# Performance work log

Hardware: AMD Instinct MI355X
Metric: run time of the kernel (lower is better)

## Reference

```python
import jax, jax.numpy as jnp
from jax import lax
from jax.experimental.ode import odeint
import numpy as np

INPUT_DIM, HIDDEN_DIM, LATENT_DIM, OUTPUT_DIM = 6, 64, 16, 1
RTOL, ATOL = 1e-3, 1e-4
NOISE_STD = 0.0  # model_noise=0 -> deterministic drift, faithful to relu(W z + b) + 0
B, T = 2048, 512


def _init(key, shape, fan_in):
    bound = 1.0 / np.sqrt(fan_in)
    return jax.random.uniform(key, shape, jnp.float32, -bound, bound)


def setup_inputs() -> dict:
    key = jax.random.key(0)
    ks = jax.random.split(key, 18)
    inp = {
        "x": jax.random.normal(ks[0], (B, T, INPUT_DIM), jnp.float32),
        # encoder GRU (input 6 -> hidden 64), torch layout: W_ih [3H, D], W_hh [3H, H]
        "enc_Wih": _init(ks[1], (3 * HIDDEN_DIM, INPUT_DIM), HIDDEN_DIM),
        "enc_Whh": _init(ks[2], (3 * HIDDEN_DIM, HIDDEN_DIM), HIDDEN_DIM),
        "enc_bih": _init(ks[3], (3 * HIDDEN_DIM,), HIDDEN_DIM),
        "enc_bhh": _init(ks[4], (3 * HIDDEN_DIM,), HIDDEN_DIM),
        "fc_mu_W": _init(ks[5], (LATENT_DIM, HIDDEN_DIM), HIDDEN_DIM),
        "fc_mu_b": _init(ks[6], (LATENT_DIM,), HIDDEN_DIM),
        "fc_lv_W": _init(ks[7], (LATENT_DIM, HIDDEN_DIM), HIDDEN_DIM),
        "fc_lv_b": _init(ks[8], (LATENT_DIM,), HIDDEN_DIM),
        # latent SDE drift linear 16 -> 16
        "ode_W": _init(ks[9], (LATENT_DIM, LATENT_DIM), LATENT_DIM),
        "ode_b": _init(ks[10], (LATENT_DIM,), LATENT_DIM),
        # decoder fc 16 -> 64, then GRU (input 64 -> hidden 1)
        "dec_fc_W": _init(ks[11], (HIDDEN_DIM, LATENT_DIM), LATENT_DIM),
        "dec_fc_b": _init(ks[12], (HIDDEN_DIM,), LATENT_DIM),
        "dec_Wih": _init(ks[13], (3 * OUTPUT_DIM, HIDDEN_DIM), OUTPUT_DIM),
        "dec_Whh": _init(ks[14], (3 * OUTPUT_DIM, OUTPUT_DIM), OUTPUT_DIM),
        "dec_bih": _init(ks[15], (3 * OUTPUT_DIM,), OUTPUT_DIM),
        "dec_bhh": _init(ks[16], (3 * OUTPUT_DIM,), OUTPUT_DIM),
    }
    return inp


def _gru_cell(h, x_gates, Whh, bhh):
    # x_gates: precomputed x @ Wih.T + bih, shape [B, 3H]; h: [B, H]
    h_gates = h @ Whh.T + bhh
    xr, xz, xn = jnp.split(x_gates, 3, axis=-1)
    hr, hz, hn = jnp.split(h_gates, 3, axis=-1)
    r = jax.nn.sigmoid(xr + hr)
    zg = jax.nn.sigmoid(xz + hz)
    n = jnp.tanh(xn + r * hn)
    return (1.0 - zg) * n + zg * h


def _forward(x, enc_Wih, enc_Whh, enc_bih, enc_bhh, fc_mu_W, fc_mu_b,
             fc_lv_W, fc_lv_b, ode_W, ode_b, dec_fc_W, dec_fc_b,
             dec_Wih, dec_Whh, dec_bih, dec_bhh):
    Bsz, Tlen, _ = x.shape
    # ---- encoder GRU, keep only last hidden state ----
    xg = jnp.einsum('btd,gd->btg', x, enc_Wih) + enc_bih  # [B,T,3H]
    h0 = jnp.zeros((Bsz, HIDDEN_DIM), x.dtype)
    def enc_step(h, xt):
        return _gru_cell(h, xt, enc_Whh, enc_bhh), None
    hT, _ = lax.scan(enc_step, h0, jnp.swapaxes(xg, 0, 1))
    mu = hT @ fc_mu_W.T + fc_mu_b          # [B,16]
    log_var = hT @ fc_lv_W.T + fc_lv_b     # [B,16]
    # deterministic reparam exactly as source: z = mu + sqrt(exp(log_var))
    z0 = mu + jnp.exp(0.5 * log_var)
    # ---- dopri5 adaptive integration of dz/dt = relu(W z + b) on t in [0,1] ----
    def drift(z, t):
        return jax.nn.relu(z @ ode_W.T + ode_b)
    ts = jnp.linspace(0.0, 1.0, 10)
    zs = odeint(drift, z0, ts, rtol=RTOL, atol=ATOL)
    z = zs[-1]                              # [B,16]
    # ---- decoder: relu(fc1), repeat over time, GRU(64->1) ----
    zd = jax.nn.relu(z @ dec_fc_W.T + dec_fc_b)            # [B,64]
    xg_dec = zd @ dec_Wih.T + dec_bih                       # same every step, [B,3]
    hd0 = jnp.zeros((Bsz, OUTPUT_DIM), x.dtype)
    def dec_step(h, _):
        h = _gru_cell(h, xg_dec, dec_Whh, dec_bhh)
        return h, h
    _, outs = lax.scan(dec_step, hd0, None, length=Tlen)    # [T,B,1]
    x_recon = jnp.swapaxes(outs, 0, 1)                      # [B,T,1]
    return x_recon, mu, log_var


def reference(x, enc_Wih, enc_Whh, enc_bih, enc_bhh, fc_mu_W, fc_mu_b,
              fc_lv_W, fc_lv_b, ode_W, ode_b, dec_fc_W, dec_fc_b,
              dec_Wih, dec_Whh, dec_bih, dec_bhh):
    return _forward(x, enc_Wih, enc_Whh, enc_bih, enc_bhh, fc_mu_W, fc_mu_b,
                    fc_lv_W, fc_lv_b, ode_W, ode_b, dec_fc_W, dec_fc_b,
                    dec_Wih, dec_Whh, dec_bih, dec_bhh)
```

## Files before the change

### kernel.cpp

```cpp
#include <hip/hip_runtime.h>
#include <math.h>

#define B_TOTAL 2048
#define T_LEN   512
#define IN_D    6
#define HID     64
#define LAT     16
#define ROWS    4
#define THREADS 256
#define ASTRIDE 104

typedef __attribute__((ext_vector_type(8))) short bfrag;
typedef __attribute__((ext_vector_type(4))) float ffrag;

#if __has_builtin(__builtin_amdgcn_exp2f)
#define EXP2F(x) __builtin_amdgcn_exp2f(x)
#else
#define EXP2F(x) exp2f(x)
#endif
#if __has_builtin(__builtin_amdgcn_rcpf)
#define RCPF(x) __builtin_amdgcn_rcpf(x)
#else
#define RCPF(x) (1.0f / (x))
#endif

__device__ __forceinline__ float fast_sigmoid(float x){
    return RCPF(1.0f + EXP2F(-1.44269504088896340736f * x));
}
__device__ __forceinline__ float fast_tanh(float x){
    return 1.0f - 2.0f * RCPF(EXP2F(2.88539008177792681472f * x) + 1.0f);
}
__device__ __forceinline__ unsigned short f2bf_rne(float f){
    unsigned u = __float_as_uint(f);
    return (unsigned short)((u + 0x7fffu + ((u >> 16) & 1u)) >> 16);
}

extern "C" __global__ void
__attribute__((amdgpu_flat_work_group_size(THREADS, THREADS), amdgpu_waves_per_eu(2, 2)))
glsde_kernel(const float* __restrict__ x,
             const float* __restrict__ eWih, const float* __restrict__ eWhh,
             const float* __restrict__ ebih, const float* __restrict__ ebhh,
             const float* __restrict__ muW,  const float* __restrict__ mub,
             const float* __restrict__ lvW,  const float* __restrict__ lvb,
             const float* __restrict__ oW,   const float* __restrict__ ob,
             const float* __restrict__ dfW,  const float* __restrict__ dfb,
             const float* __restrict__ dWih, const float* __restrict__ dWhh,
             const float* __restrict__ dbih, const float* __restrict__ dbhh,
             float* __restrict__ out)
{
    __shared__ __align__(16) unsigned short xstage[T_LEN][ROWS][8];
    __shared__ __align__(16) unsigned short Abuf[2][16][ASTRIDE];
    __shared__ float hfp[ROWS][HID];
    __shared__ float zsh[ROWS][LAT];
    __shared__ float zdsh[ROWS][HID];
    __shared__ float xgdsh[ROWS][3];

    const int tid  = threadIdx.x;
    const int wave = tid >> 6;
    const int lane = tid & 63;
    const int nloc = lane & 15;
    const int quad = lane >> 4;
    const int mA   = lane & 15;
    const int j    = wave * 16 + nloc;
    const int b0   = blockIdx.x * ROWS;

    const float S1 = 1.44269504088896340736f;
    const float S2 = 2.0f * S1;

    bfrag Br[3], Bz[3], Bnh[2], Bnx;
    {
        const float* wr  = eWhh + (size_t)(      j) * HID;
        const float* wz  = eWhh + (size_t)( 64 + j) * HID;
        const float* wn  = eWhh + (size_t)(128 + j) * HID;
        #pragma unroll
        for (int kt = 0; kt < 2; ++kt){
            const int o = kt * 32 + quad * 8;
            #pragma unroll
            for (int e = 0; e < 8; ++e){
                Br[kt][e]  = (short)f2bf_rne(wr[o+e] * S1);
                Bz[kt][e]  = (short)f2bf_rne(wz[o+e] * S1);
                Bnh[kt][e] = (short)f2bf_rne(wn[o+e] * S2);
            }
        }
        const float* ir  = eWih + (size_t)(      j) * IN_D;
        const float* iz  = eWih + (size_t)( 64 + j) * IN_D;
        const float* inn = eWih + (size_t)(128 + j) * IN_D;
        #pragma unroll
        for (int e = 0; e < 8; ++e){
            bool v = (quad == 0 && e < IN_D);
            Br[2][e] = v ? (short)f2bf_rne(ir[e]  * S1) : (short)0;
            Bz[2][e] = v ? (short)f2bf_rne(iz[e]  * S1) : (short)0;
            Bnx[e]   = v ? (short)f2bf_rne(inn[e] * S2) : (short)0;
        }
    }
    const float bias_r = (ebih[j]      + ebhh[j])      * S1;
    const float bias_z = (ebih[64 + j] + ebhh[64 + j]) * S1;
    const float bihn2  = ebih[128 + j] * S2;
    const float bhhn2  = ebhh[128 + j] * S2;

    {
        unsigned* ap = (unsigned*)Abuf;
        for (int i = tid; i < (int)(sizeof(Abuf) / 4); i += THREADS) ap[i] = 0u;
    }

    for (int idx = tid; idx < T_LEN * ROWS; idx += THREADS){
        const int tt = idx & (T_LEN - 1);
        const int bb = idx >> 9;
        const float* xr = x + (size_t)(b0 + bb) * T_LEN * IN_D + (size_t)tt * IN_D;
        const float2* p2 = (const float2*)xr;
        float2 v0 = p2[0], v1 = p2[1], v2 = p2[2];
        bfrag f;
        f[0] = (short)f2bf_rne(v0.x); f[1] = (short)f2bf_rne(v0.y);
        f[2] = (short)f2bf_rne(v1.x); f[3] = (short)f2bf_rne(v1.y);
        f[4] = (short)f2bf_rne(v2.x); f[5] = (short)f2bf_rne(v2.y);
        f[6] = 0; f[7] = 0;
        *(bfrag*)&xstage[tt][bb][0] = f;
    }
    __syncthreads();

    float hreg = 0.f;

    const unsigned short* xsp = &xstage[0][mA >> 2][0];

    bfrag Ax = *(const bfrag*)(xsp);
    const ffrag FZ = {0.f, 0.f, 0.f, 0.f};

#define GRU_STEP(bufR, bufW, T)                                                    \
    do {                                                                           \
        const unsigned short* ah_ = &bufR[mA][0];                                  \
        bfrag Ah0 = *(const bfrag*)(ah_ + 0  + quad * 8);                          \
        bfrag Ah1 = *(const bfrag*)(ah_ + 32 + quad * 8);                          \
        int tn_ = (T) + 1; if (tn_ >= T_LEN) tn_ = T_LEN - 1;                      \
        bfrag AxN = *(const bfrag*)(xsp + (size_t)tn_ * (ROWS * 8));               \
        ffrag aRx = {bias_r, 0.f, 0.f, 0.f};                                       \
        ffrag aZx = {bias_z, 0.f, 0.f, 0.f};                                       \
        ffrag aXx = {bihn2,  0.f, 0.f, 0.f};                                       \
        ffrag aR0 = FZ, aR1 = FZ, aZ0 = FZ, aZ1 = FZ;                              \
        ffrag aH0 = FZ, aH1 = FZ;                                                  \
                       \
        aRx = __builtin_amdgcn_mfma_f32_16x16x32_bf16(Ax,  Br[2],  aRx, 0,0,0);    \
        aZx = __builtin_amdgcn_mfma_f32_16x16x32_bf16(Ax,  Bz[2],  aZx, 0,0,0);    \
        aXx = __builtin_amdgcn_mfma_f32_16x16x32_bf16(Ax,  Bnx,    aXx, 0,0,0);    \
        aR0 = __builtin_amdgcn_mfma_f32_16x16x32_bf16(Ah0, Br[0],  aR0, 0,0,0);    \
        aZ0 = __builtin_amdgcn_mfma_f32_16x16x32_bf16(Ah0, Bz[0],  aZ0, 0,0,0);    \
        aH0 = __builtin_amdgcn_mfma_f32_16x16x32_bf16(Ah0, Bnh[0], aH0, 0,0,0);    \
        aR1 = __builtin_amdgcn_mfma_f32_16x16x32_bf16(Ah1, Br[1],  aR1, 0,0,0);    \
        aZ1 = __builtin_amdgcn_mfma_f32_16x16x32_bf16(Ah1, Bz[1],  aZ1, 0,0,0);    \
        aH1 = __builtin_amdgcn_mfma_f32_16x16x32_bf16(Ah1, Bnh[1], aH1, 0,0,0);    \
        float pr = aRx[0] + (aR0[0] + aR1[0]);                                     \
        float pz = aZx[0] + (aZ0[0] + aZ1[0]);                                     \
        float ph = bhhn2  + (aH0[0] + aH1[0]);                                     \
        float rg = RCPF(1.0f + EXP2F(-pr));                                        \
        float zg = RCPF(1.0f + EXP2F(-pz));                                        \
        float yy = aXx[0] + rg * ph;                                               \
        float ng = 1.0f - 2.0f * RCPF(EXP2F(yy) + 1.0f);                           \
        float hn = (1.0f - zg) * ng + zg * hreg;                                   \
        hreg = hn;                                                                 \
        bufW[quad * 4][j] = f2bf_rne(hn);                                          \
        Ax = AxN;                                                                  \
        __syncthreads();                                                           \
    } while (0)

    for (int t = 0; t < T_LEN; t += 2){
        GRU_STEP(Abuf[0], Abuf[1], t);
        GRU_STEP(Abuf[1], Abuf[0], t + 1);
    }
#undef GRU_STEP

    hfp[quad][j] = hreg;
    __syncthreads();

    const int zrow = tid >> 4, zi = tid & 15;
    float z0v = 0.0f;
    if (tid < ROWS * LAT){
        float am = mub[zi], al = lvb[zi];
        const float4* pm = (const float4*)(muW + (size_t)zi * HID);
        const float4* pq = (const float4*)(lvW + (size_t)zi * HID);
        const float4* ph = (const float4*)(&hfp[zrow][0]);
        #pragma unroll
        for (int q = 0; q < 16; ++q){
            float4 wm = pm[q], wl = pq[q], hv = ph[q];
            am += wm.x*hv.x + wm.y*hv.y + wm.z*hv.z + wm.w*hv.w;
            al += wl.x*hv.x + wl.y*hv.y + wl.z*hv.z + wl.w*hv.w;
        }
        const size_t muBase = (size_t)B_TOTAL * T_LEN;
        out[muBase + (size_t)(b0 + zrow) * LAT + zi] = am;
        out[muBase + (size_t)B_TOTAL * LAT + (size_t)(b0 + zrow) * LAT + zi] = al;
        z0v = am + __expf(0.5f * al);
    }

    if (tid < ROWS * LAT){
        float ows[16];
        {
            const float4* pw = (const float4*)(oW + (size_t)zi * LAT);
            #pragma unroll
            for (int q = 0; q < 4; ++q){
                float4 w = pw[q];
                ows[4*q+0] = w.x; ows[4*q+1] = w.y; ows[4*q+2] = w.z; ows[4*q+3] = w.w;
            }
        }
        const float obv = ob[zi];
        float z = z0v;
        const float hstep = 1.0f / 24.0f;
        for (int s = 0; s < 24; ++s){
            float y, k1, k2, k3, k4;
            y = z;
            { float acc = obv;
              #pragma unroll
              for (int jj = 0; jj < 16; ++jj){ float yj = __shfl(y, jj, 16); acc = fmaf(ows[jj], yj, acc); }
              k1 = fmaxf(acc, 0.0f); }
            y = z + 0.5f * hstep * k1;
            { float acc = obv;
              #pragma unroll
              for (int jj = 0; jj < 16; ++jj){ float yj = __shfl(y, jj, 16); acc = fmaf(ows[jj], yj, acc); }
              k2 = fmaxf(acc, 0.0f); }
            y = z + 0.5f * hstep * k2;
            { float acc = obv;
              #pragma unroll
              for (int jj = 0; jj < 16; ++jj){ float yj = __shfl(y, jj, 16); acc = fmaf(ows[jj], yj, acc); }
              k3 = fmaxf(acc, 0.0f); }
            y = z + hstep * k3;
            { float acc = obv;
              #pragma unroll
              for (int jj = 0; jj < 16; ++jj){ float yj = __shfl(y, jj, 16); acc = fmaf(ows[jj], yj, acc); }
              k4 = fmaxf(acc, 0.0f); }
            z += (hstep / 6.0f) * (k1 + 2.0f*k2 + 2.0f*k3 + k4);
        }
        zsh[zrow][zi] = z;
    }
    __syncthreads();

    for (int idx = tid; idx < ROWS * HID; idx += THREADS){
        const int row = idx >> 6, o = idx & 63;
        float acc = dfb[o];
        const float4* pw = (const float4*)(dfW + (size_t)o * LAT);
        const float4* pz = (const float4*)(&zsh[row][0]);
        #pragma unroll
        for (int q = 0; q < 4; ++q){
            float4 w = pw[q], zv = pz[q];
            acc += w.x*zv.x + w.y*zv.y + w.z*zv.z + w.w*zv.w;
        }
        zdsh[row][o] = fmaxf(acc, 0.0f);
    }
    __syncthreads();

    if (tid < ROWS * 3){
        const int row = tid / 3, gg = tid % 3;
        float acc = dbih[gg];
        const float4* pw = (const float4*)(dWih + (size_t)gg * HID);
        const float4* pz = (const float4*)(&zdsh[row][0]);
        #pragma unroll
        for (int q = 0; q < 16; ++q){
            float4 w = pw[q], zv = pz[q];
            acc += w.x*zv.x + w.y*zv.y + w.z*zv.z + w.w*zv.w;
        }
        xgdsh[row][gg] = acc;
    }
    __syncthreads();

    if (tid < ROWS){
        const int row = tid;
        const float xr = xgdsh[row][0], xz = xgdsh[row][1], xn = xgdsh[row][2];
        const float A0 = dWhh[0], A1 = dWhh[1], A2 = dWhh[2];
        const float c0 = dbhh[0], c1 = dbhh[1], c2 = dbhh[2];
        float* orow = out + (size_t)(b0 + row) * T_LEN;
        float h = 0.0f;
        float ob4[4];
        for (int t = 0; t < T_LEN; ++t){
            float rr = fast_sigmoid(xr + A0 * h + c0);
            float zz = fast_sigmoid(xz + A1 * h + c1);
            float nn = fast_tanh(xn + rr * (A2 * h + c2));
            h = (1.0f - zz) * nn + zz * h;
            ob4[t & 3] = h;
            if ((t & 3) == 3) *(float4*)(orow + (t - 3)) = *(float4*)ob4;
        }
    }
}

extern "C" void kernel_launch(void* const* d_in, const int* in_sizes, int n_in,
                              void* d_out, int out_size, void* d_ws, size_t ws_size,
                              hipStream_t stream){
    glsde_kernel<<<B_TOTAL / ROWS, THREADS, 0, stream>>>(
        (const float*)d_in[0],  (const float*)d_in[1],  (const float*)d_in[2],
        (const float*)d_in[3],  (const float*)d_in[4],  (const float*)d_in[5],
        (const float*)d_in[6],  (const float*)d_in[7],  (const float*)d_in[8],
        (const float*)d_in[9],  (const float*)d_in[10], (const float*)d_in[11],
        (const float*)d_in[12], (const float*)d_in[13], (const float*)d_in[14],
        (const float*)d_in[15], (const float*)d_in[16], (float*)d_out);
}
```

Measured before the change: 332.3 us.

## Software-pipeline input-projection MFMAs one step ahead and chain accumulators

The input-gate MFMAs for step t+1 are now issued during step t, after the hidden-state MFMAs, so they sit off the serial recurrence's critical path. The hidden MFMAs accumulate straight into the precomputed input results rather than summing separate partial accumulators, which removes the scalar adds. Odd blocks also sleep briefly before the loop to stagger phases across blocks. In exchange, the MFMAs now form dependent accumulation chains, and more accumulator registers stay live.

```diff
diff --git a/kernel.cpp b/kernel.cpp
--- a/kernel.cpp
+++ b/kernel.cpp
@@ -23,6 +23,7 @@
 #else
 #define RCPF(x) (1.0f / (x))
 #endif
+#define MFMA16(A, B, C) __builtin_amdgcn_mfma_f32_16x16x32_bf16((A), (B), (C), 0, 0, 0)
 
 __device__ __forceinline__ float fast_sigmoid(float x){
     return RCPF(1.0f + EXP2F(-1.44269504088896340736f * x));
@@ -118,41 +119,47 @@
     }
     __syncthreads();
 
+#if __has_builtin(__builtin_amdgcn_s_sleep)
+    if (blockIdx.x & 1) __builtin_amdgcn_s_sleep(7);
+#endif
+
     float hreg = 0.f;
 
     const unsigned short* xsp = &xstage[0][mA >> 2][0];
 
+    const ffrag FZ = {0.f, 0.f, 0.f, 0.f};
+    ffrag xRa = FZ, xZa = FZ, xXa = FZ, xRb = FZ, xZb = FZ, xXb = FZ;
+    ffrag aH = FZ;
+
     bfrag Ax = *(const bfrag*)(xsp);
-    const ffrag FZ = {0.f, 0.f, 0.f, 0.f};
-
-#define GRU_STEP(bufR, bufW, T)                                                    \
+    xRa[0] = bias_r; xZa[0] = bias_z; xXa[0] = bihn2;
+    xRa = MFMA16(Ax, Br[2], xRa);
+    xZa = MFMA16(Ax, Bz[2], xZa);
+    xXa = MFMA16(Ax, Bnx,   xXa);
+    Ax = *(const bfrag*)(xsp + (size_t)1 * (ROWS * 8));
+
+#define GRU_STEP(bufR, bufW, xR, xZ, xX, xRn, xZn, xXn, T)                         \
     do {                                                                           \
         const unsigned short* ah_ = &bufR[mA][0];                                  \
         bfrag Ah0 = *(const bfrag*)(ah_ + 0  + quad * 8);                          \
         bfrag Ah1 = *(const bfrag*)(ah_ + 32 + quad * 8);                          \
-        int tn_ = (T) + 1; if (tn_ >= T_LEN) tn_ = T_LEN - 1;                      \
+        ffrag aR = MFMA16(Ah0, Br[0],  xR);                                        \
+        ffrag aZ = MFMA16(Ah0, Bz[0],  xZ);                                        \
+        aH[0] = bhhn2;                                                             \
+        aH = MFMA16(Ah0, Bnh[0], aH);                                              \
+        aR = MFMA16(Ah1, Br[1],  aR);                                              \
+        aZ = MFMA16(Ah1, Bz[1],  aZ);                                              \
+        aH = MFMA16(Ah1, Bnh[1], aH);                                              \
+                  \
+        xRn[0] = bias_r; xZn[0] = bias_z; xXn[0] = bihn2;                          \
+        xRn = MFMA16(Ax, Br[2], xRn);                                              \
+        xZn = MFMA16(Ax, Bz[2], xZn);                                              \
+        xXn = MFMA16(Ax, Bnx,   xXn);                                              \
+        int tn_ = (T) + 2; if (tn_ > T_LEN - 1) tn_ = T_LEN - 1;                   \
         bfrag AxN = *(const bfrag*)(xsp + (size_t)tn_ * (ROWS * 8));               \
-        ffrag aRx = {bias_r, 0.f, 0.f, 0.f};                                       \
-        ffrag aZx = {bias_z, 0.f, 0.f, 0.f};                                       \
-        ffrag aXx = {bihn2,  0.f, 0.f, 0.f};                                       \
-        ffrag aR0 = FZ, aR1 = FZ, aZ0 = FZ, aZ1 = FZ;                              \
-        ffrag aH0 = FZ, aH1 = FZ;                                                  \
-                       \
-        aRx = __builtin_amdgcn_mfma_f32_16x16x32_bf16(Ax,  Br[2],  aRx, 0,0,0);    \
-        aZx = __builtin_amdgcn_mfma_f32_16x16x32_bf16(Ax,  Bz[2],  aZx, 0,0,0);    \
-        aXx = __builtin_amdgcn_mfma_f32_16x16x32_bf16(Ax,  Bnx,    aXx, 0,0,0);    \
-        aR0 = __builtin_amdgcn_mfma_f32_16x16x32_bf16(Ah0, Br[0],  aR0, 0,0,0);    \
-        aZ0 = __builtin_amdgcn_mfma_f32_16x16x32_bf16(Ah0, Bz[0],  aZ0, 0,0,0);    \
-        aH0 = __builtin_amdgcn_mfma_f32_16x16x32_bf16(Ah0, Bnh[0], aH0, 0,0,0);    \
-        aR1 = __builtin_amdgcn_mfma_f32_16x16x32_bf16(Ah1, Br[1],  aR1, 0,0,0);    \
-        aZ1 = __builtin_amdgcn_mfma_f32_16x16x32_bf16(Ah1, Bz[1],  aZ1, 0,0,0);    \
-        aH1 = __builtin_amdgcn_mfma_f32_16x16x32_bf16(Ah1, Bnh[1], aH1, 0,0,0);    \
-        float pr = aRx[0] + (aR0[0] + aR1[0]);                                     \
-        float pz = aZx[0] + (aZ0[0] + aZ1[0]);                                     \
-        float ph = bhhn2  + (aH0[0] + aH1[0]);                                     \
-        float rg = RCPF(1.0f + EXP2F(-pr));                                        \
-        float zg = RCPF(1.0f + EXP2F(-pz));                                        \
-        float yy = aXx[0] + rg * ph;                                               \
+        float rg = RCPF(1.0f + EXP2F(-aR[0]));                                     \
+        float zg = RCPF(1.0f + EXP2F(-aZ[0]));                                     \
+        float yy = xX[0] + rg * aH[0];                                             \
         float ng = 1.0f - 2.0f * RCPF(EXP2F(yy) + 1.0f);                           \
         float hn = (1.0f - zg) * ng + zg * hreg;                                   \
         hreg = hn;                                                                 \
@@ -162,8 +169,8 @@
     } while (0)
 
     for (int t = 0; t < T_LEN; t += 2){
-        GRU_STEP(Abuf[0], Abuf[1], t);
-        GRU_STEP(Abuf[1], Abuf[0], t + 1);
+        GRU_STEP(Abuf[0], Abuf[1], xRa, xZa, xXa, xRb, xZb, xXb, t);
+        GRU_STEP(Abuf[1], Abuf[0], xRb, xZb, xXb, xRa, xZa, xXa, t + 1);
     }
 #undef GRU_STEP
 
```

Result: faster. 323.2 us (-2.8%).
